# Optimization experiments

Hardware: AMD Instinct MI355X
Metric: run time of the kernel (lower is better)

## Reference

```python
import jax, jax.numpy as jnp
import numpy as np

V, D, T_BLK, H, L = 32000, 1024, 1024, 8 * 2, 8
HD = D // H
B, T = 4, 1024
EPS = 1e-5


def _ln(x, g, b):
    mu = jnp.mean(x, axis=-1, keepdims=True)
    var = jnp.mean(jnp.square(x - mu), axis=-1, keepdims=True)
    return (x - mu) * jax.lax.rsqrt(var + EPS) * g + b


def _forward(idx, tok_emb, pos_emb, Wq, Wk, Wv, Wo, bo, ln1_g, ln1_b, ln2_g, ln2_b,
             W1, b1, W2, b2, lnf_g, lnf_b, Whead, bhead):
    Bc, Tc = idx.shape
    x = tok_emb[idx] + pos_emb[:Tc]          # [B,T,D]
    mask = jnp.tril(jnp.ones((Tc, Tc), dtype=bool))
    scale = HD ** -0.5

    def block(x, p):
        wq, wk, wv, wo, bo_, g1, be1, g2, be2, w1, bf1, w2, bf2 = p
        xn = _ln(x, g1, be1)
        # per-head no-bias projections: wq/wk/wv are [H, D, HD]
        q = jnp.einsum('btd,hde->bhte', xn, wq)
        k = jnp.einsum('btd,hde->bhte', xn, wk)
        v = jnp.einsum('btd,hde->bhte', xn, wv)
        scores = jnp.einsum('bhte,bhse->bhts', q, k) * scale
        scores = jnp.where(mask, scores, -jnp.inf)
        w = jax.nn.softmax(scores, axis=-1)
        o = jnp.einsum('bhts,bhse->bhte', w, v)             # [B,H,T,HD]
        o = o.transpose(0, 2, 1, 3).reshape(Bc, Tc, D)       # concat heads
        x = x + jnp.einsum('btd,de->bte', o, wo) + bo_
        xn2 = _ln(x, g2, be2)
        h = jax.nn.gelu(jnp.einsum('btd,df->btf', xn2, w1) + bf1, approximate=False)
        x = x + jnp.einsum('btf,fd->btd', h, w2) + bf2
        return x, None

    x, _ = jax.lax.scan(block, x, (Wq, Wk, Wv, Wo, bo, ln1_g, ln1_b, ln2_g, ln2_b,
                                   W1, b1, W2, b2))
    x = _ln(x, lnf_g, lnf_b)
    logits = jnp.einsum('btd,dv->btv', x, Whead) + bhead
    return logits


def setup_inputs() -> dict:
    key = jax.random.key(0)
    ks = jax.random.split(key, 16)
    s = 0.02
    inp = {
        'idx': jax.random.randint(ks[0], (B, T), 0, V),
        'tok_emb': jax.random.normal(ks[1], (V, D), jnp.float32) * s,
        'pos_emb': jax.random.normal(ks[2], (T_BLK, D), jnp.float32) * s,
        'Wq': jax.random.normal(ks[3], (L, H, D, HD), jnp.float32) * s,
        'Wk': jax.random.normal(ks[4], (L, H, D, HD), jnp.float32) * s,
        'Wv': jax.random.normal(ks[5], (L, H, D, HD), jnp.float32) * s,
        'Wo': jax.random.normal(ks[6], (L, D, D), jnp.float32) * s,
        'bo': jnp.zeros((L, D), jnp.float32),
        'ln1_g': jnp.ones((L, D), jnp.float32),
        'ln1_b': jnp.zeros((L, D), jnp.float32),
        'ln2_g': jnp.ones((L, D), jnp.float32),
        'ln2_b': jnp.zeros((L, D), jnp.float32),
        'W1': jax.random.normal(ks[7], (L, D, 4 * D), jnp.float32) * s,
        'b1': jnp.zeros((L, 4 * D), jnp.float32),
        'W2': jax.random.normal(ks[8], (L, 4 * D, D), jnp.float32) * s,
        'b2': jnp.zeros((L, D), jnp.float32),
        'lnf_g': jnp.ones((D,), jnp.float32),
        'lnf_b': jnp.zeros((D,), jnp.float32),
        'Whead': jax.random.normal(ks[9], (D, V), jnp.float32) * s,
        'bhead': jnp.zeros((V,), jnp.float32),
    }
    return inp


def reference(idx, tok_emb, pos_emb, Wq, Wk, Wv, Wo, bo, ln1_g, ln1_b, ln2_g, ln2_b,
              W1, b1, W2, b2, lnf_g, lnf_b, Whead, bhead):
    return _forward(idx, tok_emb, pos_emb, Wq, Wk, Wv, Wo, bo, ln1_g, ln1_b,
                    ln2_g, ln2_b, W1, b1, W2, b2, lnf_g, lnf_b, Whead, bhead)
```

## Files before the change

kernel.cpp:

```cpp
#include <hip/hip_runtime.h>
#include <hip/hip_bf16.h>

typedef short bf16x8 __attribute__((ext_vector_type(8)));
typedef float f32x4 __attribute__((ext_vector_type(4)));

__device__ __forceinline__ unsigned short f2bf(float f) {
  union { float f; unsigned u; } un; un.f = f;
  unsigned r = un.u + 0x7fffu + ((un.u >> 16) & 1u);
  return (unsigned short)(r >> 16);
}

__device__ __forceinline__ void gl_lds16(const void* g, void* l) {
  __builtin_amdgcn_global_load_lds(
      (const __attribute__((address_space(1))) void*)g,
      (__attribute__((address_space(3))) void*)l, 16, 0, 0);
}

__global__ __launch_bounds__(256) void embed_k(const int* __restrict__ idx,
                                               const float* __restrict__ tok,
                                               const float* __restrict__ pos,
                                               float* __restrict__ x) {
  int m = blockIdx.x, t = threadIdx.x;
  int tk = idx[m];
  int tp = m & 1023;
  f32x4 a = __builtin_nontemporal_load((const f32x4*)(tok + (long)tk * 1024) + t);
  f32x4 p = ((const f32x4*)(pos + (long)tp * 1024))[t];
  a += p;
  ((f32x4*)(x + (long)m * 1024))[t] = a;
}

__global__ __launch_bounds__(256) void ln_k(const float* __restrict__ x,
                                            const float* __restrict__ g,
                                            const float* __restrict__ b,
                                            unsigned short* __restrict__ out) {
  int row = blockIdx.x, t = threadIdx.x;
  float4 v = ((const float4*)(x + (long)row * 1024))[t];
  float s = v.x + v.y + v.z + v.w;
  float ss = v.x * v.x + v.y * v.y + v.z * v.z + v.w * v.w;
#pragma unroll
  for (int d = 32; d; d >>= 1) { s += __shfl_xor(s, d, 64); ss += __shfl_xor(ss, d, 64); }
  __shared__ float red[8];
  int wave = t >> 6, lane = t & 63;
  if (lane == 0) { red[wave] = s; red[wave + 4] = ss; }
  __syncthreads();
  s = red[0] + red[1] + red[2] + red[3];
  ss = red[4] + red[5] + red[6] + red[7];
  float mu = s * (1.f / 1024.f);
  float var = ss * (1.f / 1024.f) - mu * mu;
  float rstd = rsqrtf(var + 1e-5f);
  float4 gv = ((const float4*)g)[t];
  float4 bv = ((const float4*)b)[t];
  ushort4 o;
  o.x = f2bf((v.x - mu) * rstd * gv.x + bv.x);
  o.y = f2bf((v.y - mu) * rstd * gv.y + bv.y);
  o.z = f2bf((v.z - mu) * rstd * gv.z + bv.z);
  o.w = f2bf((v.w - mu) * rstd * gv.w + bv.w);
  ((ushort4*)(out + (long)row * 1024))[t] = o;
}

__global__ __launch_bounds__(256) void tr_k(const float* __restrict__ in,
                                            unsigned short* __restrict__ out,
                                            int R, int C, long inStride, long outStride) {
  __shared__ float tile[32][33];
  int batch = blockIdx.z;
  int c0 = blockIdx.x * 32, r0 = blockIdx.y * 32;
  const float* ip = in + (long)batch * inStride;
  unsigned short* op = out + (long)batch * outStride;
  int tx = threadIdx.x, ty = threadIdx.y;
#pragma unroll
  for (int i = 0; i < 4; ++i)
    tile[ty + i * 8][tx] = __builtin_nontemporal_load(ip + (long)(r0 + ty + i * 8) * C + c0 + tx);
  __syncthreads();
#pragma unroll
  for (int i = 0; i < 4; ++i)
    op[(long)(c0 + ty + i * 8) * R + r0 + tx] = f2bf(tile[tx][ty + i * 8]);
}

__global__ __launch_bounds__(256) void tr_qkv_k(const float* __restrict__ wq,
                                                const float* __restrict__ wk,
                                                const float* __restrict__ wv,
                                                unsigned short* __restrict__ out) {
  __shared__ float tile[32][33];
  int z = blockIdx.z;
  int tsel = z >> 7, rem = z & 127;
  int l = rem >> 4, h = rem & 15;
  const float* ip = (tsel == 0 ? wq : tsel == 1 ? wk : wv) + (long)rem * 65536;
  unsigned short* op = out + (long)l * (3072 * 1024) + (long)tsel * (1024 * 1024) +
                       (long)h * 65536;
  int c0 = blockIdx.x * 32, r0 = blockIdx.y * 32;
  int tx = threadIdx.x, ty = threadIdx.y;
#pragma unroll
  for (int i = 0; i < 4; ++i)
    tile[ty + i * 8][tx] = __builtin_nontemporal_load(ip + (long)(r0 + ty + i * 8) * 64 + c0 + tx);
  __syncthreads();
#pragma unroll
  for (int i = 0; i < 4; ++i)
    op[(long)(c0 + ty + i * 8) * 1024 + r0 + tx] = f2bf(tile[tx][ty + i * 8]);
}

template <int EPI>
__global__ __launch_bounds__(256) void gemm_bt(const unsigned short* __restrict__ A,
                                               const unsigned short* __restrict__ Bt,
                                               float* __restrict__ outf,
                                               unsigned short* __restrict__ outb,
                                               const float* __restrict__ bias,
                                               const float* __restrict__ res,
                                               int M, int N, int K) {
  __shared__ __align__(16) unsigned short sA[128 * 64];
  __shared__ __align__(16) unsigned short sB[128 * 64];
  const int t = threadIdx.x;
  const int wave = t >> 6, lane = t & 63;

  const int gx = gridDim.x, gy = gridDim.y;
  const int nwg = gx * gy;
  const int bid = blockIdx.y * gx + blockIdx.x;
  const int qd = nwg >> 3, rd = nwg & 7;
  const int xcd = bid & 7, off = bid >> 3;
  const int swz = (xcd < rd ? xcd * (qd + 1) : rd * (qd + 1) + (xcd - rd) * qd) + off;
  const int m0 = (swz % gy) << 7, n0 = (swz / gy) << 7;

  const int wm = (wave >> 1) * 64, wn = (wave & 1) * 64;
  const f32x4 z4 = {0.f, 0.f, 0.f, 0.f};
  f32x4 acc[4][4];
#pragma unroll
  for (int i = 0; i < 4; ++i)
#pragma unroll
    for (int j = 0; j < 4; ++j) acc[i][j] = z4;

  const int srow = t >> 3;
  const int scb = (((t & 7) ^ ((t >> 3) & 7)) << 4);
  const char* Ab = (const char*)A;
  const char* Bb = (const char*)Bt;
  char* sAb = (char*)sA;
  char* sBb = (char*)sB;
  const long ldb2 = (long)K * 2;
  const int pc0 = (((lane >> 4) ^ (lane & 7)) << 4);

  for (int k0 = 0; k0 < K; k0 += 64) {
    __syncthreads();
#pragma unroll
    for (int i = 0; i < 4; ++i) {
      int row = i * 32 + srow;
      gl_lds16(Ab + (long)(m0 + row) * ldb2 + (long)k0 * 2 + scb,
               sAb + i * 4096 + wave * 1024);
      gl_lds16(Bb + (long)(n0 + row) * ldb2 + (long)k0 * 2 + scb,
               sBb + i * 4096 + wave * 1024);
    }
    __syncthreads();
#pragma unroll
    for (int kk = 0; kk < 2; ++kk) {
      const int kb = pc0 ^ (kk << 6);
      bf16x8 af[4], bfr[4];
#pragma unroll
      for (int f = 0; f < 4; ++f) {
        int ra = wm + f * 16 + (lane & 15);
        af[f] = *(const bf16x8*)(sAb + ra * 128 + kb);
        int rb = wn + f * 16 + (lane & 15);
        bfr[f] = *(const bf16x8*)(sBb + rb * 128 + kb);
      }
#pragma unroll
      for (int fm = 0; fm < 4; ++fm)
#pragma unroll
        for (int fn = 0; fn < 4; ++fn)
          acc[fm][fn] = __builtin_amdgcn_mfma_f32_16x16x32_bf16(af[fm], bfr[fn], acc[fm][fn], 0, 0, 0);
    }
  }
  const int rl = (lane >> 4) << 2;
  const int cl = lane & 15;
#pragma unroll
  for (int fm = 0; fm < 4; ++fm) {
#pragma unroll
    for (int fn = 0; fn < 4; ++fn) {
#pragma unroll
      for (int r = 0; r < 4; ++r) {
        int m = m0 + wm + fm * 16 + rl + r;
        int n = n0 + wn + fn * 16 + cl;
        float v = acc[fm][fn][r];
        if (EPI == 1) v += bias[n] + res[(long)m * N + n];
        if (EPI == 1) outf[(long)m * N + n] = v;
        else outb[(long)m * N + n] = f2bf(v);
      }
    }
  }
}

template <int EPI>
__global__ __launch_bounds__(512, 1) void gemm256(const unsigned short* __restrict__ A,
                                                  const unsigned short* __restrict__ Bt,
                                                  float* __restrict__ outf,
                                                  unsigned short* __restrict__ outb,
                                                  const float* __restrict__ bias,
                                                  int M, int N, int K) {
  __shared__ __align__(16) char smem[131072];
  const int t = threadIdx.x;
  const int wave = t >> 6, lane = t & 63;

  const int gx = gridDim.x, gy = gridDim.y;
  const int nwg = gx * gy;
  const int bid = blockIdx.y * gx + blockIdx.x;
  const int qd = nwg >> 3, rd = nwg & 7;
  const int xcd = bid & 7, off = bid >> 3;
  const int swz = (xcd < rd ? xcd * (qd + 1) : rd * (qd + 1) + (xcd - rd) * qd) + off;
  const int m0 = (swz % gy) << 8, n0 = (swz / gy) << 8;

  const int wm = (wave >> 2) << 7;
  const int wn = (wave & 3) << 6;
  const int KT = K >> 5;

  const f32x4 z4 = {0.f, 0.f, 0.f, 0.f};
  f32x4 acc[8][4];
#pragma unroll
  for (int i = 0; i < 8; ++i)
#pragma unroll
    for (int j = 0; j < 4; ++j) acc[i][j] = z4;

  const int srow = t >> 2;
  const int sck = (((t & 3) ^ ((t >> 3) & 3)) << 4);
  const long ldb = (long)K * 2;
  const char* Asrc = (const char*)A + (long)(m0 + srow) * ldb + sck;
  const char* Asrc2 = Asrc + 128 * ldb;
  const char* Bsrc = (const char*)Bt + (long)(n0 + srow) * ldb + sck;
  const char* Bsrc2 = Bsrc + 128 * ldb;

#define STAGE_A(tt)                                                     \
  { char* d = smem + ((tt) & 3) * 32768 + wave * 1024;                  \
    long ko = (long)(tt) * 64;                                          \
    gl_lds16(Asrc + ko, d); gl_lds16(Asrc2 + ko, d + 8192); }
#define STAGE_B(tt)                                                     \
  { char* d = smem + ((tt) & 3) * 32768 + 16384 + wave * 1024;          \
    long ko = (long)(tt) * 64;                                          \
    gl_lds16(Bsrc + ko, d); gl_lds16(Bsrc2 + ko, d + 8192); }

  STAGE_A(0); STAGE_B(0);
  STAGE_A(1); STAGE_B(1);
  STAGE_A(2); STAGE_B(2);
  asm volatile("s_waitcnt vmcnt(8)" ::: "memory");
  __builtin_amdgcn_sched_barrier(0);
  __builtin_amdgcn_s_barrier();

  const int pck16 = (((lane >> 4) ^ ((lane >> 1) & 3)) << 4);
  const int la15 = lane & 15;

  for (int tt = 0; tt < KT; ++tt) {
    const char* bA = smem + (tt & 3) * 32768;
    const char* bB = bA + 16384;
    bf16x8 af[4], af2[4], bfr[4];

#pragma unroll
    for (int f = 0; f < 4; ++f)
      af[f] = *(const bf16x8*)(bA + (wm + f * 16 + la15) * 64 + pck16);
#pragma unroll
    for (int g = 0; g < 4; ++g)
      bfr[g] = *(const bf16x8*)(bB + (wn + g * 16 + la15) * 64 + pck16);
    if (tt + 3 < KT) STAGE_A(tt + 3);
    __builtin_amdgcn_s_setprio(1);
#pragma unroll
    for (int fm = 0; fm < 4; ++fm)
#pragma unroll
      for (int fn = 0; fn < 4; ++fn)
        acc[fm][fn] = __builtin_amdgcn_mfma_f32_16x16x32_bf16(af[fm], bfr[fn], acc[fm][fn], 0, 0, 0);
    __builtin_amdgcn_s_setprio(0);

#pragma unroll
    for (int f = 0; f < 4; ++f)
      af2[f] = *(const bf16x8*)(bA + (wm + (f + 4) * 16 + la15) * 64 + pck16);
    if (tt + 3 < KT) STAGE_B(tt + 3);
    __builtin_amdgcn_s_setprio(1);
#pragma unroll
    for (int fm = 0; fm < 4; ++fm)
#pragma unroll
      for (int fn = 0; fn < 4; ++fn)
        acc[fm + 4][fn] = __builtin_amdgcn_mfma_f32_16x16x32_bf16(af2[fm], bfr[fn], acc[fm + 4][fn], 0, 0, 0);
    __builtin_amdgcn_s_setprio(0);

    if (tt + 1 < KT) {
      if (tt + 3 < KT)      asm volatile("s_waitcnt vmcnt(8)" ::: "memory");
      else if (tt + 2 < KT) asm volatile("s_waitcnt vmcnt(4)" ::: "memory");
      else                  asm volatile("s_waitcnt vmcnt(0)" ::: "memory");
      __builtin_amdgcn_sched_barrier(0);
    }
    __builtin_amdgcn_s_barrier();
  }
#undef STAGE_A
#undef STAGE_B

  const int rl = (lane >> 4) << 2;
#pragma unroll
  for (int fm = 0; fm < 8; ++fm) {
#pragma unroll
    for (int fn = 0; fn < 4; ++fn) {
#pragma unroll
      for (int r = 0; r < 4; ++r) {
        int m = m0 + wm + fm * 16 + rl + r;
        int n = n0 + wn + fn * 16 + la15;
        float v = acc[fm][fn][r];
        if (EPI == 2 || EPI == 3) v += bias[n];
        if (EPI == 2) v = 0.5f * v * (1.f + erff(v * 0.70710678118f));
        if (EPI == 3) {
          __builtin_nontemporal_store(v, outf + (long)m * N + n);
        } else {
          outb[(long)m * N + n] = f2bf(v);
        }
      }
    }
  }
}

__global__ __launch_bounds__(256) void attn_k(const unsigned short* __restrict__ qkv,
                                              unsigned short* __restrict__ o) {
  const int qt = blockIdx.x;
  const int pair = blockIdx.y;
  const int b = pair >> 4, h = pair & 15;
  const int t = threadIdx.x, wave = t >> 6, lane = t & 63;
  __shared__ __align__(16) unsigned short sQ[64 * 64];
  __shared__ __align__(16) unsigned short sK[2][64 * 64];
  __shared__ __align__(16) unsigned short sV[2][64 * 64];
  __shared__ __align__(16) unsigned short sP[4][16 * 64];

  const long baseq = (long)b * (1024 * 3072) + (long)h * 64;
  const unsigned short* qp = qkv + baseq;
  const unsigned short* kp = qkv + baseq + 1024;
  const unsigned short* vp = qkv + baseq + 2048;
  const long baseo = (long)b * (1024 * 1024) + (long)h * 64;

  const int row0 = t >> 3, c0 = t & 7;
  const int row1 = (t + 256) >> 3, c1 = t & 7;
  const int qoff0 = ((c0 ^ (row0 & 7)) << 3);
  const int qoff1 = ((c1 ^ (row1 & 7)) << 3);

  gl_lds16(qp + (long)(qt * 64 + row0) * 3072 + qoff0, (char*)sQ + wave * 1024);
  gl_lds16(qp + (long)(qt * 64 + row1) * 3072 + qoff1, (char*)sQ + 4096 + wave * 1024);
  gl_lds16(kp + (long)(0 + row0) * 3072 + qoff0, (char*)sK[0] + wave * 1024);
  gl_lds16(kp + (long)(0 + row1) * 3072 + qoff1, (char*)sK[0] + 4096 + wave * 1024);
  bf16x8 vr0 = *(const bf16x8*)(vp + (long)row0 * 3072 + (c0 << 3));
  bf16x8 vr1 = *(const bf16x8*)(vp + (long)row1 * 3072 + (c1 << 3));
  {
    char* vb = (char*)sV[0];
#pragma unroll
    for (int j = 0; j < 8; ++j) {
      int e0 = (c0 << 3) + j, e1 = (c1 << 3) + j;
      *(unsigned short*)(vb + e0 * 128 + ((row0 * 2) ^ ((e0 & 7) << 4))) = (unsigned short)vr0[j];
      *(unsigned short*)(vb + e1 * 128 + ((row1 * 2) ^ ((e1 & 7) << 4))) = (unsigned short)vr1[j];
    }
  }
  __syncthreads();

  float lst[4] = {0.f, 0.f, 0.f, 0.f};
  const f32x4 z4 = {0.f, 0.f, 0.f, 0.f};
  f32x4 oacc[4];
#pragma unroll
  for (int eb = 0; eb < 4; ++eb) oacc[eb] = z4;

  const int qrow = wave * 16 + (lane & 15);
  const int qswz0 = ((lane >> 4) << 4) ^ ((qrow & 7) << 4);
  const int prow = lane & 15;

  for (int kt = 0; kt <= qt; ++kt) {
    const int cur = kt & 1;

    bf16x8 aq[2];
#pragma unroll
    for (int kk = 0; kk < 2; ++kk)
      aq[kk] = *(const bf16x8*)((char*)sQ + qrow * 128 + ((kk << 6) ^ qswz0));
    f32x4 sf[4];
#pragma unroll
    for (int cb = 0; cb < 4; ++cb) {
      f32x4 s = z4;
      int kr = cb * 16 + (lane & 15);
      int kswz = ((kr & 7) << 4);
#pragma unroll
      for (int kk = 0; kk < 2; ++kk) {
        int e0 = (kk * 32 + ((lane >> 4) << 3)) * 2;
        bf16x8 bk = *(const bf16x8*)((char*)sK[cur] + kr * 128 + (e0 ^ kswz));
        s = __builtin_amdgcn_mfma_f32_16x16x32_bf16(aq[kk], bk, s, 0, 0, 0);
      }
      sf[cb] = s;
    }

    if (kt < qt) {
      const int nxt = cur ^ 1;
      const long krb = (long)((kt + 1) * 64);
      gl_lds16(kp + (krb + row0) * 3072 + qoff0, (char*)sK[nxt] + wave * 1024);
      gl_lds16(kp + (krb + row1) * 3072 + qoff1, (char*)sK[nxt] + 4096 + wave * 1024);
      vr0 = *(const bf16x8*)(vp + (krb + row0) * 3072 + (c0 << 3));
      vr1 = *(const bf16x8*)(vp + (krb + row1) * 3072 + (c1 << 3));
    }

    const bool diag = (kt == qt);
    unsigned short* pb = sP[wave];
#pragma unroll
    for (int r = 0; r < 4; ++r) {
      int qg = wave * 16 + ((lane >> 4) << 2) + r;
      int lr = ((lane >> 4) << 2) + r;
      float rs = 0.f;
#pragma unroll
      for (int cb = 0; cb < 4; ++cb) {
        float p;
        if (diag) {
          int kg = cb * 16 + (lane & 15);
          p = (kg > qg) ? 0.f : __expf(sf[cb][r] * 0.125f);
        } else {
          p = __expf(sf[cb][r] * 0.125f);
        }
        rs += p;
        int col = cb * 16 + (lane & 15);
        *(unsigned short*)((char*)pb + lr * 128 + ((col * 2) ^ ((lr & 7) << 4))) = f2bf(p);
      }
      lst[r] += rs;
    }

    bf16x8 ap[2];
#pragma unroll
    for (int kk = 0; kk < 2; ++kk) {
      int j0 = (kk * 32 + ((lane >> 4) << 3)) * 2;
      ap[kk] = *(const bf16x8*)((char*)pb + prow * 128 + (j0 ^ ((prow & 7) << 4)));
    }
#pragma unroll
    for (int eb = 0; eb < 4; ++eb) {
      int er = eb * 16 + (lane & 15);
      int eswz = ((er & 7) << 4);
#pragma unroll
      for (int kk = 0; kk < 2; ++kk) {
        int j0 = (kk * 32 + ((lane >> 4) << 3)) * 2;
        bf16x8 bv = *(const bf16x8*)((char*)sV[cur] + er * 128 + (j0 ^ eswz));
        oacc[eb] = __builtin_amdgcn_mfma_f32_16x16x32_bf16(ap[kk], bv, oacc[eb], 0, 0, 0);
      }
    }

    if (kt < qt) {
      char* vb = (char*)sV[cur ^ 1];
#pragma unroll
      for (int j = 0; j < 8; ++j) {
        int e0 = (c0 << 3) + j, e1 = (c1 << 3) + j;
        *(unsigned short*)(vb + e0 * 128 + ((row0 * 2) ^ ((e0 & 7) << 4))) = (unsigned short)vr0[j];
        *(unsigned short*)(vb + e1 * 128 + ((row1 * 2) ^ ((e1 & 7) << 4))) = (unsigned short)vr1[j];
      }
      __syncthreads();
    }
  }

#pragma unroll
  for (int r = 0; r < 4; ++r) {
#pragma unroll
    for (int d = 1; d < 16; d <<= 1) lst[r] += __shfl_xor(lst[r], d, 64);
    float inv = 1.f / lst[r];
    int qg = qt * 64 + wave * 16 + ((lane >> 4) << 2) + r;
#pragma unroll
    for (int eb = 0; eb < 4; ++eb) {
      int e = eb * 16 + (lane & 15);
      o[baseo + (long)qg * 1024 + e] = f2bf(oacc[eb][r] * inv);
    }
  }
}

extern "C" void kernel_launch(void* const* d_in, const int* in_sizes, int n_in,
                              void* d_out, int out_size, void* d_ws, size_t ws_size,
                              hipStream_t stream) {
  const int* idx = (const int*)d_in[0];
  const float* tok = (const float*)d_in[1];
  const float* pos = (const float*)d_in[2];
  const float* Wq = (const float*)d_in[3];
  const float* Wk = (const float*)d_in[4];
  const float* Wv = (const float*)d_in[5];
  const float* Wo = (const float*)d_in[6];
  const float* bo = (const float*)d_in[7];
  const float* ln1g = (const float*)d_in[8];
  const float* ln1b = (const float*)d_in[9];
  const float* ln2g = (const float*)d_in[10];
  const float* ln2b = (const float*)d_in[11];
  const float* W1 = (const float*)d_in[12];
  const float* b1 = (const float*)d_in[13];
  const float* W2 = (const float*)d_in[14];
  const float* b2 = (const float*)d_in[15];
  const float* lnfg = (const float*)d_in[16];
  const float* lnfb = (const float*)d_in[17];
  const float* Wh = (const float*)d_in[18];
  const float* bh = (const float*)d_in[19];

  char* ws = (char*)d_ws;
  const long Mi = 1024 * 1024;
  float* x = (float*)ws;
  unsigned short* xn = (unsigned short*)(ws + 16 * Mi);
  unsigned short* qkv = (unsigned short*)(ws + 24 * Mi);
  unsigned short* ob = (unsigned short*)(ws + 48 * Mi);
  unsigned short* hmid = (unsigned short*)(ws + 24 * Mi);
  unsigned short* wqkvT = (unsigned short*)(ws + 56 * Mi);
  unsigned short* wot = (unsigned short*)(ws + 104 * Mi);
  unsigned short* w1t = (unsigned short*)(ws + 106 * Mi);
  unsigned short* w2t = (unsigned short*)(ws + 114 * Mi);
  unsigned short* whT = (unsigned short*)(ws + 56 * Mi);

  dim3 blk256(256), blk512(512), blkT(32, 8);

  embed_k<<<4096, blk256, 0, stream>>>(idx, tok, pos, x);
  tr_qkv_k<<<dim3(2, 32, 384), blkT, 0, stream>>>(Wq, Wk, Wv, wqkvT);

  for (int l = 0; l < 8; ++l) {
    const float* wo_l = Wo + (long)l * 1048576;
    const float* w1_l = W1 + (long)l * 4194304;
    const float* w2_l = W2 + (long)l * 4194304;
    const float* bo_l = bo + (long)l * 1024;
    const float* b1_l = b1 + (long)l * 4096;
    const float* b2_l = b2 + (long)l * 1024;
    const unsigned short* wqkv_l = wqkvT + (long)l * (3072 * 1024);

    tr_k<<<dim3(32, 32, 1), blkT, 0, stream>>>(wo_l, wot, 1024, 1024, 0, 0);
    tr_k<<<dim3(128, 32, 1), blkT, 0, stream>>>(w1_l, w1t, 1024, 4096, 0, 0);
    tr_k<<<dim3(32, 128, 1), blkT, 0, stream>>>(w2_l, w2t, 4096, 1024, 0, 0);

    ln_k<<<4096, blk256, 0, stream>>>(x, ln1g + l * 1024, ln1b + l * 1024, xn);

    gemm256<0><<<dim3(12, 16), blk512, 0, stream>>>(xn, wqkv_l, nullptr, qkv, nullptr, 4096, 3072, 1024);

    attn_k<<<dim3(16, 64), blk256, 0, stream>>>(qkv, ob);

    gemm_bt<1><<<dim3(8, 32), blk256, 0, stream>>>(ob, wot, x, nullptr, bo_l, x, 4096, 1024, 1024);

    ln_k<<<4096, blk256, 0, stream>>>(x, ln2g + l * 1024, ln2b + l * 1024, xn);

    gemm256<2><<<dim3(16, 16), blk512, 0, stream>>>(xn, w1t, nullptr, hmid, b1_l, 4096, 4096, 1024);
    gemm_bt<1><<<dim3(8, 32), blk256, 0, stream>>>(hmid, w2t, x, nullptr, b2_l, x, 4096, 1024, 4096);
  }

  ln_k<<<4096, blk256, 0, stream>>>(x, lnfg, lnfb, xn);
  tr_k<<<dim3(1000, 32, 1), blkT, 0, stream>>>(Wh, whT, 1024, 32000, 0, 0);
  gemm256<3><<<dim3(125, 16), blk512, 0, stream>>>(xn, whT, (float*)d_out, nullptr, bh, 4096, 32000, 1024);
}
```

Before: 2.594 ms.

## Restructure GEMM main loop to 64-wide K tiles with double buffering and 8-phase schedule

The bf16 GEMM main loop now stages K=64 per tile (128-byte rows, 8-way XOR swizzle) into two 64KB LDS buffers, replacing the earlier four 32-wide buffers. Global-to-LDS loads are split into half-tile chunks interleaved across four per-quarter phases, each separated by barriers and lgkm waits, and MFMAs are issued in quarter groups. The aim is to cut barrier and LDS-read overhead per unit of MFMA work and to overlap global loads with compute more finely. The cost is many more barriers per tile and more fragile vmcnt bookkeeping; K must be a multiple of 128.

Result: no change. 2.595 ms (+0.0%).

```diff
diff --git a/kernel.cpp b/kernel.cpp
--- a/kernel.cpp
+++ b/kernel.cpp
@@ -205,7 +205,7 @@
 
   const int wm = (wave >> 2) << 7;
   const int wn = (wave & 3) << 6;
-  const int KT = K >> 5;
+  const int KT2 = K >> 7;
 
   const f32x4 z4 = {0.f, 0.f, 0.f, 0.f};
   f32x4 acc[8][4];
@@ -214,84 +214,111 @@
 #pragma unroll
     for (int j = 0; j < 4; ++j) acc[i][j] = z4;
 
-  const int srow = t >> 2;
-  const int sck = (((t & 3) ^ ((t >> 3) & 3)) << 4);
+  const int sck = (((t & 7) ^ ((t >> 3) & 7)) << 4);
   const long ldb = (long)K * 2;
-  const char* Asrc = (const char*)A + (long)(m0 + srow) * ldb + sck;
-  const char* Asrc2 = Asrc + 128 * ldb;
-  const char* Bsrc = (const char*)Bt + (long)(n0 + srow) * ldb + sck;
-  const char* Bsrc2 = Bsrc + 128 * ldb;
-
-#define STAGE_A(tt)                                                     \
-  { char* d = smem + ((tt) & 3) * 32768 + wave * 1024;                  \
-    long ko = (long)(tt) * 64;                                          \
-    gl_lds16(Asrc + ko, d); gl_lds16(Asrc2 + ko, d + 8192); }
-#define STAGE_B(tt)                                                     \
-  { char* d = smem + ((tt) & 3) * 32768 + 16384 + wave * 1024;          \
-    long ko = (long)(tt) * 64;                                          \
-    gl_lds16(Bsrc + ko, d); gl_lds16(Bsrc2 + ko, d + 8192); }
-
-  STAGE_A(0); STAGE_B(0);
-  STAGE_A(1); STAGE_B(1);
-  STAGE_A(2); STAGE_B(2);
-  asm volatile("s_waitcnt vmcnt(8)" ::: "memory");
+  const char* Abase = (const char*)A + (long)(m0 + (t >> 3)) * ldb + sck;
+  const char* Bbase = (const char*)Bt + (long)(n0 + (t >> 3)) * ldb + sck;
+
+#define STG(base, tt, h, boff)                                              \
+  { char* d = smem + (((tt) & 1) << 16) + (boff) + ((h) << 14) + wave * 1024; \
+    const char* s = (base) + (long)((h) * 128) * ldb + ((long)(tt) << 7);     \
+    gl_lds16(s, d); gl_lds16(s + (ldb << 6), d + 8192); }
+
+  STG(Bbase, 0, 0, 32768); STG(Bbase, 0, 1, 32768);
+  STG(Abase, 0, 0, 0);     STG(Abase, 0, 1, 0);
+  STG(Bbase, 1, 0, 32768); STG(Bbase, 1, 1, 32768);
+  STG(Abase, 1, 0, 0);
+  asm volatile("s_waitcnt vmcnt(6)" ::: "memory");
   __builtin_amdgcn_sched_barrier(0);
   __builtin_amdgcn_s_barrier();
 
-  const int pck16 = (((lane >> 4) ^ ((lane >> 1) & 3)) << 4);
   const int la15 = lane & 15;
-
-  for (int tt = 0; tt < KT; ++tt) {
-    const char* bA = smem + (tt & 3) * 32768;
-    const char* bB = bA + 16384;
-    bf16x8 af[4], af2[4], bfr[4];
-
-#pragma unroll
-    for (int f = 0; f < 4; ++f)
-      af[f] = *(const bf16x8*)(bA + (wm + f * 16 + la15) * 64 + pck16);
-#pragma unroll
-    for (int g = 0; g < 4; ++g)
-      bfr[g] = *(const bf16x8*)(bB + (wn + g * 16 + la15) * 64 + pck16);
-    if (tt + 3 < KT) STAGE_A(tt + 3);
-    __builtin_amdgcn_s_setprio(1);
-#pragma unroll
-    for (int fm = 0; fm < 4; ++fm)
-#pragma unroll
-      for (int fn = 0; fn < 4; ++fn)
-        acc[fm][fn] = __builtin_amdgcn_mfma_f32_16x16x32_bf16(af[fm], bfr[fn], acc[fm][fn], 0, 0, 0);
-    __builtin_amdgcn_s_setprio(0);
-
-#pragma unroll
-    for (int f = 0; f < 4; ++f)
-      af2[f] = *(const bf16x8*)(bA + (wm + (f + 4) * 16 + la15) * 64 + pck16);
-    if (tt + 3 < KT) STAGE_B(tt + 3);
-    __builtin_amdgcn_s_setprio(1);
-#pragma unroll
-    for (int fm = 0; fm < 4; ++fm)
-#pragma unroll
-      for (int fn = 0; fn < 4; ++fn)
-        acc[fm + 4][fn] = __builtin_amdgcn_mfma_f32_16x16x32_bf16(af2[fm], bfr[fn], acc[fm + 4][fn], 0, 0, 0);
-    __builtin_amdgcn_s_setprio(0);
-
-    if (tt + 1 < KT) {
-      if (tt + 3 < KT)      asm volatile("s_waitcnt vmcnt(8)" ::: "memory");
-      else if (tt + 2 < KT) asm volatile("s_waitcnt vmcnt(4)" ::: "memory");
-      else                  asm volatile("s_waitcnt vmcnt(0)" ::: "memory");
-      __builtin_amdgcn_sched_barrier(0);
-    }
-    __builtin_amdgcn_s_barrier();
-  }
-#undef STAGE_A
-#undef STAGE_B
+  const int pck0 = (((lane >> 4) ^ (la15 & 7)) << 4);
+  const int pck1 = pck0 ^ 64;
+
+#define DS_A(q)                                                              \
+  a00 = *(const bf16x8*)(bA + (wm + ((q) * 2) * 16 + la15) * 128 + pck0);    \
+  a01 = *(const bf16x8*)(bA + (wm + ((q) * 2) * 16 + la15) * 128 + pck1);    \
+  a10 = *(const bf16x8*)(bA + (wm + ((q) * 2 + 1) * 16 + la15) * 128 + pck0);\
+  a11 = *(const bf16x8*)(bA + (wm + ((q) * 2 + 1) * 16 + la15) * 128 + pck1);
+
+#define MFMA_Q(q)                                                                              \
+  __builtin_amdgcn_s_setprio(1);                                                               \
+  { _Pragma("unroll") for (int nf = 0; nf < 4; ++nf) {                                         \
+      acc[(q)*2][nf]     = __builtin_amdgcn_mfma_f32_16x16x32_bf16(a00, bfr[nf][0], acc[(q)*2][nf], 0, 0, 0);     \
+      acc[(q)*2][nf]     = __builtin_amdgcn_mfma_f32_16x16x32_bf16(a01, bfr[nf][1], acc[(q)*2][nf], 0, 0, 0);     \
+      acc[(q)*2 + 1][nf] = __builtin_amdgcn_mfma_f32_16x16x32_bf16(a10, bfr[nf][0], acc[(q)*2 + 1][nf], 0, 0, 0); \
+      acc[(q)*2 + 1][nf] = __builtin_amdgcn_mfma_f32_16x16x32_bf16(a11, bfr[nf][1], acc[(q)*2 + 1][nf], 0, 0, 0); \
+  } }                                                                                          \
+  __builtin_amdgcn_s_setprio(0);
+
+#define BAR_LGKM()                                    \
+  __builtin_amdgcn_s_barrier();                       \
+  asm volatile("s_waitcnt lgkmcnt(0)" ::: "memory");  \
+  __builtin_amdgcn_sched_barrier(0);
+
+  for (int it = 0; it < KT2; ++it) {
+    const bool more = (it + 1 < KT2);
+#pragma unroll
+    for (int g = 0; g < 2; ++g) {
+      const int tt = 2 * it + g;
+      const char* bA = smem + ((tt & 1) << 16);
+      const char* bB = bA + 32768;
+      bf16x8 bfr[4][2], a00, a01, a10, a11;
+
+#pragma unroll
+      for (int nf = 0; nf < 4; ++nf) {
+        bfr[nf][0] = *(const bf16x8*)(bB + (wn + nf * 16 + la15) * 128 + pck0);
+        bfr[nf][1] = *(const bf16x8*)(bB + (wn + nf * 16 + la15) * 128 + pck1);
+      }
+      DS_A(0);
+      if (g == 0) { STG(Abase, tt + 1, 1, 0); }
+      else if (more) { STG(Abase, tt + 1, 1, 0); }
+      asm volatile("s_waitcnt lgkmcnt(8)" ::: "memory");
+      BAR_LGKM();
+      MFMA_Q(0);
+      __builtin_amdgcn_s_barrier();
+
+      DS_A(1);
+      if (more) { STG(Bbase, tt + 2, 0, 32768); }
+      BAR_LGKM();
+      MFMA_Q(1);
+      __builtin_amdgcn_s_barrier();
+
+      DS_A(2);
+      if (more) { STG(Bbase, tt + 2, 1, 32768); }
+      BAR_LGKM();
+      MFMA_Q(2);
+      __builtin_amdgcn_s_barrier();
+
+      DS_A(3);
+      if (more) { STG(Abase, tt + 2, 0, 0); }
+      BAR_LGKM();
+      MFMA_Q(3);
+      if (g == 0) {
+        if (more) { asm volatile("s_waitcnt vmcnt(6)" ::: "memory"); }
+        else      { asm volatile("s_waitcnt vmcnt(0)" ::: "memory"); }
+        __builtin_amdgcn_sched_barrier(0);
+      } else if (more) {
+        asm volatile("s_waitcnt vmcnt(6)" ::: "memory");
+        __builtin_amdgcn_sched_barrier(0);
+      }
+      __builtin_amdgcn_s_barrier();
+    }
+  }
+#undef STG
+#undef DS_A
+#undef MFMA_Q
+#undef BAR_LGKM
 
   const int rl = (lane >> 4) << 2;
 #pragma unroll
   for (int fm = 0; fm < 8; ++fm) {
 #pragma unroll
-    for (int fn = 0; fn < 4; ++fn) {
-#pragma unroll
-      for (int r = 0; r < 4; ++r) {
-        int m = m0 + wm + fm * 16 + rl + r;
+    for (int r = 0; r < 4; ++r) {
+      int m = m0 + wm + fm * 16 + rl + r;
+#pragma unroll
+      for (int fn = 0; fn < 4; ++fn) {
         int n = n0 + wn + fn * 16 + la15;
         float v = acc[fm][fn][r];
         if (EPI == 2 || EPI == 3) v += bias[n];
```
